# Performance work log

Measured on AMD Instinct MI355X. Metric: run time of the kernel, lower is better.

## Reference

```python
import jax, jax.numpy as jnp
import numpy as np

B = 4; C = 3; IMG = 256; P = 16; HP = 16; HW = 256
DIM = 512; DEPTH = 6; HEADS = 8; DH = 64
NS = 50; SH = 4; SDH = 64; ITERS = 3; RPD = 128; FF = 2048; N = NS + HW


def _ln(x, g, b):
    m = jnp.mean(x, -1, keepdims=True)
    v = jnp.var(x, -1, keepdims=True)
    return (x - m) * jax.lax.rsqrt(v + 1e-5) * g + b


def _rms(x, g):
    # lucidrains RMSNorm: F.normalize(x, dim=-1) * sqrt(dim) * gamma
    n = jnp.linalg.norm(x, axis=-1, keepdims=True)
    return x / jnp.maximum(n, 1e-12) * (DIM ** 0.5) * g


def setup_inputs() -> dict:
    key = jax.random.key(0)
    ks = iter(jax.random.split(key, 64))
    def W(*s):
        return jax.random.normal(next(ks), s, jnp.float32) * 0.02
    SI = SH * SDH
    d = {}
    d['images'] = jax.random.normal(next(ks), (B, C, IMG, IMG), jnp.float32)
    d['slot_noise'] = jax.random.normal(next(ks), (B, NS, DIM), jnp.float32)
    d['patch_w'] = W(C * P * P, DIM); d['patch_b'] = jnp.zeros((DIM,))
    d['hpos'] = W(HP, DIM); d['wpos'] = W(HP, DIM)
    d['rp_w1'] = W(2, RPD); d['rp_b1'] = jnp.zeros((RPD,))
    d['rp_w2'] = W(RPD, RPD); d['rp_b2'] = jnp.zeros((RPD,))
    d['rp_w3'] = W(RPD, HEADS); d['rp_b3'] = jnp.zeros((HEADS,))
    d['slots_mu'] = W(1, 1, DIM); d['slots_logsigma'] = jnp.zeros((1, 1, DIM))
    d['sa_ln_in_g'] = jnp.ones((DIM,)); d['sa_ln_in_b'] = jnp.zeros((DIM,))
    d['sa_ln_sl_g'] = jnp.ones((DIM,)); d['sa_ln_sl_b'] = jnp.zeros((DIM,))
    d['sa_wq'] = W(DIM, SI); d['sa_bq'] = jnp.zeros((SI,))
    d['sa_wk'] = W(DIM, SI); d['sa_bk'] = jnp.zeros((SI,))
    d['sa_wv'] = W(DIM, SI); d['sa_bv'] = jnp.zeros((SI,))
    d['sa_wo'] = W(SI, DIM); d['sa_bo'] = jnp.zeros((DIM,))
    d['gru_wih'] = W(DIM, 3 * DIM); d['gru_whh'] = W(DIM, 3 * DIM)
    d['gru_bih'] = jnp.zeros((3 * DIM,)); d['gru_bhh'] = jnp.zeros((3 * DIM,))
    d['sa_ln_ff_g'] = jnp.ones((DIM,)); d['sa_ln_ff_b'] = jnp.zeros((DIM,))
    d['sa_mlp_w1'] = W(DIM, DIM); d['sa_mlp_b1'] = jnp.zeros((DIM,))
    d['sa_mlp_w2'] = W(DIM, DIM); d['sa_mlp_b2'] = jnp.zeros((DIM,))
    d['s2c_w'] = W(DIM, 2); d['s2c_b'] = jnp.zeros((2,))
    d['attn_g'] = jnp.ones((DEPTH, DIM))
    d['wq'] = W(DEPTH, DIM, HEADS * DH); d['wk'] = W(DEPTH, DIM, HEADS * DH)
    d['wv'] = W(DEPTH, DIM, HEADS * DH); d['wo'] = W(DEPTH, HEADS * DH, DIM)
    d['ff_g'] = jnp.ones((DEPTH, DIM))
    d['ff_w1'] = W(DEPTH, DIM, FF); d['ff_b1'] = jnp.zeros((DEPTH, FF))
    d['ff_w2'] = W(DEPTH, FF, DIM); d['ff_b2'] = jnp.zeros((DEPTH, DIM))
    d['final_g'] = jnp.ones((DIM,))
    d['pred_w'] = W(DIM, DIM); d['pred_b'] = jnp.zeros((DIM,))
    return d


def reference(images, slot_noise, patch_w, patch_b, hpos, wpos,
              rp_w1, rp_b1, rp_w2, rp_b2, rp_w3, rp_b3,
              slots_mu, slots_logsigma, sa_ln_in_g, sa_ln_in_b, sa_ln_sl_g, sa_ln_sl_b,
              sa_wq, sa_bq, sa_wk, sa_bk, sa_wv, sa_bv, sa_wo, sa_bo,
              gru_wih, gru_whh, gru_bih, gru_bhh, sa_ln_ff_g, sa_ln_ff_b,
              sa_mlp_w1, sa_mlp_b1, sa_mlp_w2, sa_mlp_b2, s2c_w, s2c_b,
              attn_g, wq, wk, wv, wo, ff_g, ff_w1, ff_b1, ff_w2, ff_b2,
              final_g, pred_w, pred_b):
    b = images.shape[0]
    # patchify: b c (h p1) (w p2) -> b h w (p1 p2 c)
    x = images.reshape(b, C, HP, P, HP, P).transpose(0, 2, 4, 3, 5, 1).reshape(b, HP, HP, P * P * C)
    tokens = x @ patch_w + patch_b                     # [b, HP, HP, DIM]
    tokens = tokens + hpos[:, None, :] + wpos[None, :, :]
    tokens = tokens.reshape(b, HW, DIM)
    # --- multi-head slot attention ---
    inp = _ln(tokens, sa_ln_in_g, sa_ln_in_b)
    k = (inp @ sa_wk + sa_bk).reshape(b, HW, SH, SDH).transpose(0, 2, 1, 3)
    v = (inp @ sa_wv + sa_bv).reshape(b, HW, SH, SDH).transpose(0, 2, 1, 3)
    slots = slots_mu + jnp.exp(slots_logsigma) * slot_noise  # [b, NS, DIM]
    scale = SDH ** -0.5
    for _ in range(ITERS):
        prev = slots
        s = _ln(slots, sa_ln_sl_g, sa_ln_sl_b)
        q = (s @ sa_wq + sa_bq).reshape(b, NS, SH, SDH).transpose(0, 2, 1, 3)
        dots = jnp.einsum('bhid,bhjd->bhij', q, k) * scale     # [b, SH, NS, HW]
        attn = jax.nn.softmax(dots, axis=-2) + 1e-8            # softmax over slots
        attn = attn / jnp.sum(attn, -1, keepdims=True)         # weighted mean over inputs
        upd = jnp.einsum('bhij,bhjd->bhid', attn, v)
        upd = upd.transpose(0, 2, 1, 3).reshape(b, NS, SH * SDH) @ sa_wo + sa_bo
        # GRUCell(updates, prev_slots)
        gx = upd @ gru_wih + gru_bih
        gh = prev @ gru_whh + gru_bhh
        xr, xz, xn = jnp.split(gx, 3, -1)
        hr, hz, hn = jnp.split(gh, 3, -1)
        r = jax.nn.sigmoid(xr + hr)
        z = jax.nn.sigmoid(xz + hz)
        nn_ = jnp.tanh(xn + r * hn)
        slots = (1 - z) * nn_ + z * prev
        slots = slots + (jax.nn.relu(_ln(slots, sa_ln_ff_g, sa_ln_ff_b) @ sa_mlp_w1 + sa_mlp_b1) @ sa_mlp_w2 + sa_mlp_b2)
    objects = slots
    slot_coords = objects @ s2c_w + s2c_b              # [b, NS, 2]
    # --- relative position MLP bias (slots coords + patch grid) ---
    g = jnp.arange(HP, dtype=jnp.float32)
    grid = jnp.stack(jnp.meshgrid(g, g, indexing='ij'), -1).reshape(HW, 2)
    coords = jnp.concatenate([slot_coords, jnp.broadcast_to(grid, (b, HW, 2))], axis=1)  # [b, N, 2]
    rel = coords[:, :, None, :] - coords[:, None, :, :]   # [b, N, N, 2]
    hmid = jax.nn.silu(rel @ rp_w1 + rp_b1)
    hmid = jax.nn.silu(hmid @ rp_w2 + rp_b2)
    bias = jnp.transpose(hmid @ rp_w3 + rp_b3, (0, 3, 1, 2))  # [b, HEADS, N, N]
    # --- transformer with per-layer rel-pos bias ---
    x = jnp.concatenate([objects, tokens], axis=1)     # [b, N, DIM]
    ascale = DH ** -0.5
    for l in range(DEPTH):
        h = _rms(x, attn_g[l])
        qh = (h @ wq[l]).reshape(b, N, HEADS, DH).transpose(0, 2, 1, 3)
        kh = (h @ wk[l]).reshape(b, N, HEADS, DH).transpose(0, 2, 1, 3)
        vh = (h @ wv[l]).reshape(b, N, HEADS, DH).transpose(0, 2, 1, 3)
        sim = jnp.einsum('bhid,bhjd->bhij', qh, kh) * ascale + bias
        a = jax.nn.softmax(sim, -1)
        o = jnp.einsum('bhij,bhjd->bhid', a, vh).transpose(0, 2, 1, 3).reshape(b, N, HEADS * DH) @ wo[l]
        x = x + o
        h = _rms(x, ff_g[l])
        x = x + (jax.nn.gelu(h @ ff_w1[l] + ff_b1[l]) @ ff_w2[l] + ff_b2[l])
    x = _rms(x, final_g)
    return x[:, NS:] @ pred_w + pred_b                 # [b, HW, DIM]
```

## Files before the change

### kernel.cpp

```cpp
#include <hip/hip_runtime.h>
#include <hip/hip_bf16.h>

typedef __hip_bfloat16 bf16;
typedef short short8v __attribute__((ext_vector_type(8)));
typedef float float4v __attribute__((ext_vector_type(4)));

static __device__ __forceinline__ float b2f(bf16 x){ return __bfloat162float(x); }

static __device__ __forceinline__ float ldin(const void* p, size_t i, bool isbf) {
  return isbf ? b2f(((const bf16*)p)[i]) : ((const float*)p)[i];
}

static __device__ __forceinline__ unsigned short f2bu(float f) {
  bf16 h = __float2bfloat16(f);
  return *reinterpret_cast<unsigned short*>(&h);
}

#define CDIV(a,b) (((a)+(b)-1)/(b))

#define NB   4
#define NSL  50
#define HWT  256
#define NT   306
#define DIM  512
#define NH   8
#define FF   2048
#define RPP  28100
#define PCH  56200

static __device__ __forceinline__ void rp_decode(int q, int& i, int& j) {
  if (q < 15300) { i = q / NT; j = q % NT; }
  else { int r = q - 15300; i = NSL + r / NSL; j = r % NSL; }
}

__global__ void detect_k(const void* p, int* flag) {
  const unsigned short* u = (const unsigned short*)p;
  int t = threadIdx.x;
  int e = (u[t] >> 7) & 0xFF;
  __shared__ int anybad;
  if (t == 0) anybad = 0;
  __syncthreads();
  if (e >= 0x88) atomicOr(&anybad, 1);
  __syncthreads();
  if (t == 0) *flag = anybad ? 0 : 1;
}

struct WtArgs {
  const void* W[17];
  unsigned long long wto[17];
  int K[17], N[17];
  int base[18];
};

__global__ __launch_bounds__(256) void wtrans_all_k(WtArgs a, unsigned short* __restrict__ WT,
                                                    const int* __restrict__ flagp) {
  const bool isbf = *flagp != 0;
  int bid = blockIdx.x;
  int idx = 0;
#pragma unroll
  for (int i = 1; i < 17; ++i) if (bid >= a.base[i]) idx = i;
  int t0 = bid - a.base[idx];
  const int K = a.K[idx], N = a.N[idx];
  const int tilesN = N >> 6;
  const int perLayer = tilesN * (K >> 6);
  const int layer = t0 / perLayer, rem = t0 % perLayer;
  const int n0 = (rem % tilesN) * 64, k0 = (rem / tilesN) * 64;
  const void* W = a.W[idx];
  unsigned short* dst0 = WT + a.wto[idx];
  const size_t slice = (size_t)K * N * layer;

  __shared__ unsigned short S[64 * 72];
  int t = threadIdx.x;
  int kk = t >> 4, nn = (t & 15) * 4;
#pragma unroll
  for (int r = 0; r < 4; ++r) {
    int k = k0 + kk + r * 16;
    unsigned short v[4];
    if (isbf) {
      ushort4 u = *(const ushort4*)((const unsigned short*)W + slice + (size_t)k * N + n0 + nn);
      v[0]=u.x; v[1]=u.y; v[2]=u.z; v[3]=u.w;
    } else {
      float4 f = *(const float4*)((const float*)W + slice + (size_t)k * N + n0 + nn);
      v[0]=f2bu(f.x); v[1]=f2bu(f.y); v[2]=f2bu(f.z); v[3]=f2bu(f.w);
    }
#pragma unroll
    for (int i = 0; i < 4; ++i) S[(nn + i) * 72 + kk + r * 16] = v[i];
  }
  __syncthreads();
  int nr = t >> 2, kc = (t & 3) * 16;
  short8v s0 = *(const short8v*)&S[nr * 72 + kc];
  short8v s1 = *(const short8v*)&S[nr * 72 + kc + 8];
  unsigned short* dst = dst0 + slice + (size_t)(n0 + nr) * K + k0 + kc;
  *(short8v*)dst = s0;
  *(short8v*)(dst + 8) = s1;
}

#define LDK 72
static __device__ __forceinline__ void gemm_body2(
    const void* __restrict__ A, int aty,
    const unsigned short* __restrict__ WT,
    const void* __restrict__ bias, size_t boff,
    void* __restrict__ C, int oty,
    int M, int N, int K, int kbeg, int kend,
    int act, int mode, int spec,
    const void* __restrict__ p0, const void* __restrict__ p1,
    bool isbf)
{
  __shared__ unsigned short As[64 * LDK];
  __shared__ unsigned short Bs[64 * LDK];
  const int tid = threadIdx.x;
  const int lane = tid & 63, wave = tid >> 6;
  const int quad = lane >> 4, ti = lane & 15;
  const int wm = (wave & 1) * 32, wn = (wave >> 1) * 32;
  const int bm = blockIdx.y * 64, bn = blockIdx.x * 64;
  const int srow = tid >> 2, sch = (tid & 3) * 16;

  unsigned short ha[16], hb[16];
  const int gm = bm + srow;
  const bool aok = gm < M;
  const unsigned short* Abf = (const unsigned short*)A + (size_t)gm * K;
  const float*          Af  = (const float*)A + (size_t)gm * K;
  const unsigned short* Bp  = WT + (size_t)(bn + srow) * K;

  auto fetchA = [&](int k0) {
    if (aok) {
      if (aty) {
        const ushort4* ap = (const ushort4*)(Abf + k0 + sch);
#pragma unroll
        for (int i = 0; i < 4; ++i) {
          ushort4 u = ap[i];
          ha[i*4+0]=u.x; ha[i*4+1]=u.y; ha[i*4+2]=u.z; ha[i*4+3]=u.w;
        }
      } else {
        const float4* ap = (const float4*)(Af + k0 + sch);
#pragma unroll
        for (int i = 0; i < 4; ++i) {
          float4 f = ap[i];
          ha[i*4+0]=f2bu(f.x); ha[i*4+1]=f2bu(f.y); ha[i*4+2]=f2bu(f.z); ha[i*4+3]=f2bu(f.w);
        }
      }
    } else {
#pragma unroll
      for (int i = 0; i < 16; ++i) ha[i] = 0;
    }
  };
  auto fetchB = [&](int k0) {
    const ushort4* bp = (const ushort4*)(Bp + k0 + sch);
#pragma unroll
    for (int i = 0; i < 4; ++i) {
      ushort4 u = bp[i];
      hb[i*4+0]=u.x; hb[i*4+1]=u.y; hb[i*4+2]=u.z; hb[i*4+3]=u.w;
    }
  };

  float4v acc00 = {0,0,0,0}, acc01 = {0,0,0,0}, acc10 = {0,0,0,0}, acc11 = {0,0,0,0};
  fetchA(kbeg); fetchB(kbeg);
  for (int k0 = kbeg; k0 < kend; k0 += 64) {
    *(short8v*)&As[srow * LDK + sch]     = *(short8v*)ha;
    *(short8v*)&As[srow * LDK + sch + 8] = *(short8v*)(ha + 8);
    *(short8v*)&Bs[srow * LDK + sch]     = *(short8v*)hb;
    *(short8v*)&Bs[srow * LDK + sch + 8] = *(short8v*)(hb + 8);
    __syncthreads();
    if (k0 + 64 < kend) { fetchA(k0 + 64); fetchB(k0 + 64); }
#pragma unroll
    for (int ks = 0; ks < 2; ++ks) {
      short8v a0 = *reinterpret_cast<const short8v*>(&As[(wm + ti)      * LDK + ks * 32 + quad * 8]);
      short8v a1 = *reinterpret_cast<const short8v*>(&As[(wm + 16 + ti) * LDK + ks * 32 + quad * 8]);
      short8v b0 = *reinterpret_cast<const short8v*>(&Bs[(wn + ti)      * LDK + ks * 32 + quad * 8]);
      short8v b1 = *reinterpret_cast<const short8v*>(&Bs[(wn + 16 + ti) * LDK + ks * 32 + quad * 8]);
      acc00 = __builtin_amdgcn_mfma_f32_16x16x32_bf16(a0, b0, acc00, 0, 0, 0);
      acc01 = __builtin_amdgcn_mfma_f32_16x16x32_bf16(a0, b1, acc01, 0, 0, 0);
      acc10 = __builtin_amdgcn_mfma_f32_16x16x32_bf16(a1, b0, acc10, 0, 0, 0);
      acc11 = __builtin_amdgcn_mfma_f32_16x16x32_bf16(a1, b1, acc11, 0, 0, 0);
    }
    __syncthreads();
  }

  float4v accs[2][2] = {{acc00, acc01}, {acc10, acc11}};
#pragma unroll
  for (int mi = 0; mi < 2; ++mi) {
#pragma unroll
    for (int ni = 0; ni < 2; ++ni) {
      int row0 = bm + wm + mi * 16 + quad * 4;
      int col  = bn + wn + ni * 16 + ti;
      float bv = (bias && kbeg == 0) ? ldin(bias, boff + col, isbf) : 0.f;
#pragma unroll
      for (int r = 0; r < 4; ++r) {
        int row = row0 + r;
        if (row >= M) continue;
        float v = accs[mi][ni][r] + bv;
        if (act == 1) v = fmaxf(v, 0.f);
        else if (act == 2) {
          float u = 0.7978845608028654f * (v + 0.044715f * v * v * v);
          v = 0.5f * v * (1.f + tanhf(u));
        } else if (act == 3) {
          v = v / (1.f + expf(-v));
        }
        if (spec == 2 && kbeg == 0) {
          int hh = (row >> 4) & 15, ww = row & 15;
          v += ldin(p0, hh * N + col, isbf) + ldin(p1, ww * N + col, isbf);
        }
        if (spec == 1) {
          int b_ = row / NT, n_ = row % NT;
          if (n_ >= NSL) {
            size_t oi = ((size_t)(b_ * HWT + (n_ - NSL))) * N + col;
            if (isbf) ((bf16*)C)[oi] = __float2bfloat16(v);
            else      ((float*)C)[oi] = v;
          }
        } else {
          size_t idx = (size_t)row * N + col;
          if (oty) ((bf16*)C)[idx] = __float2bfloat16(v);
          else {
            float* Cf = (float*)C;
            if (mode == 2) atomicAdd(&Cf[idx], v);
            else if (mode == 1) Cf[idx] += v;
            else Cf[idx] = v;
          }
        }
      }
    }
  }
}

__global__ __launch_bounds__(256) void gemm_mfma(
    const void* A, int aty, const unsigned short* WT, size_t woff,
    const void* bias, size_t boff, void* C, int oty,
    int M, int N, int K, int act, int accum, int zsplit,
    int spec, const void* p0, const void* p1, const int* __restrict__ flagp)
{
  int ksz = K / zsplit;
  int kbeg = blockIdx.z * ksz;
  int mode = zsplit > 1 ? 2 : (accum ? 1 : 0);
  gemm_body2(A, aty, WT + woff, bias, boff, C, oty, M, N, K, kbeg, kbeg + ksz,
             act, mode, spec, p0, p1, *flagp != 0);
}

__global__ __launch_bounds__(256) void gemm_mfma_tri(
    const void* A, int aty, const unsigned short* WT, size_t o0, size_t o1, size_t o2,
    void* C0, void* C1, void* C2, int oty, int M, int N, int K,
    const int* __restrict__ flagp)
{
  size_t o = blockIdx.z == 0 ? o0 : (blockIdx.z == 1 ? o1 : o2);
  void* C = blockIdx.z == 0 ? C0 : (blockIdx.z == 1 ? C1 : C2);
  gemm_body2(A, aty, WT + o, nullptr, 0, C, oty, M, N, K, 0, K, 0, 0, 0,
             nullptr, nullptr, *flagp != 0);
}

__global__ __launch_bounds__(256) void gemm_mfma_duo(
    const void* A0, const void* A1, int aty, const unsigned short* WT, size_t o0, size_t o1,
    const void* bias0, const void* bias1, void* C0, void* C1, int oty,
    int M, int N, int K, const int* __restrict__ flagp)
{
  const void* A = blockIdx.z ? A1 : A0;
  size_t o = blockIdx.z ? o1 : o0;
  const void* bias = blockIdx.z ? bias1 : bias0;
  void* C = blockIdx.z ? C1 : C0;
  gemm_body2(A, aty, WT + o, bias, 0, C, oty, M, N, K, 0, K, 0, 0, 0,
             nullptr, nullptr, *flagp != 0);
}

__global__ void coords_k(const float* __restrict__ slots, const void* __restrict__ w,
                         const void* __restrict__ bv, float* __restrict__ coords,
                         const int* __restrict__ flagp) {
  const bool isbf = *flagp != 0;
  __shared__ float r0[256], r1[256];
  int blk = blockIdx.x, t = threadIdx.x;
  if (blk < 200) {
    int b = blk / 50, n = blk % 50;
    const float* x = slots + (size_t)blk * DIM;
    float v0 = x[t], v1 = x[t + 256];
    float a0 = v0 * ldin(w, 2 * t, isbf)     + v1 * ldin(w, 2 * (t + 256), isbf);
    float a1 = v0 * ldin(w, 2 * t + 1, isbf) + v1 * ldin(w, 2 * (t + 256) + 1, isbf);
    r0[t] = a0; r1[t] = a1;
    __syncthreads();
    for (int o = 128; o > 0; o >>= 1) {
      if (t < o) { r0[t] += r0[t + o]; r1[t] += r1[t + o]; }
      __syncthreads();
    }
    if (t == 0) {
      coords[((size_t)b * NT + n) * 2]     = r0[0] + ldin(bv, 0, isbf);
      coords[((size_t)b * NT + n) * 2 + 1] = r1[0] + ldin(bv, 1, isbf);
    }
  } else {
#pragma unroll
    for (int s = 0; s < 4; ++s) {
      int i = t + 256 * s;
      int b = i >> 8, tt = i & 255;
      coords[((size_t)b * NT + NSL + tt) * 2]     = (float)(tt >> 4);
      coords[((size_t)b * NT + NSL + tt) * 2 + 1] = (float)(tt & 15);
    }
  }
}

__global__ void patchify_k(const void* __restrict__ img, unsigned short* __restrict__ xp,
                           const int* __restrict__ flagp) {
  const bool isbf = *flagp != 0;
  int i = blockIdx.x * 256 + threadIdx.x;
  if (i >= NB * HWT * 768) return;
  int col = i % 768, row = i / 768;
  int c = col % 3, p2 = (col / 3) & 15, p1 = col / 48;
  int w = row & 15, h = (row >> 4) & 15, b = row >> 8;
  xp[i] = f2bu(ldin(img, (((size_t)(b * 3 + c) * 256 + h * 16 + p1) * 256) + w * 16 + p2, isbf));
}

__global__ void ln512_k(const float* __restrict__ X, const void* __restrict__ g,
                        const void* __restrict__ b, unsigned short* __restrict__ Y,
                        const int* __restrict__ flagp) {
  const bool isbf = *flagp != 0;
  int row = blockIdx.x, t = threadIdx.x;
  const float* x = X + (size_t)row * DIM;
  float v0 = x[t], v1 = x[t + 256];
  __shared__ float rs[256], rq[256];
  rs[t] = v0 + v1; rq[t] = v0 * v0 + v1 * v1;
  __syncthreads();
  for (int o = 128; o > 0; o >>= 1) {
    if (t < o) { rs[t] += rs[t + o]; rq[t] += rq[t + o]; }
    __syncthreads();
  }
  float mean = rs[0] * (1.f / 512.f);
  float var  = rq[0] * (1.f / 512.f) - mean * mean;
  float inv  = rsqrtf(var + 1e-5f);
  unsigned short* y = Y + (size_t)row * DIM;
  y[t]       = f2bu((v0 - mean) * inv * ldin(g, t, isbf)       + ldin(b, t, isbf));
  y[t + 256] = f2bu((v1 - mean) * inv * ldin(g, t + 256, isbf) + ldin(b, t + 256, isbf));
}

__global__ void rms512_k(const float* __restrict__ X, const void* __restrict__ g,
                         int goff, unsigned short* __restrict__ Y, const int* __restrict__ flagp) {
  const bool isbf = *flagp != 0;
  int row = blockIdx.x, t = threadIdx.x;
  const float* x = X + (size_t)row * DIM;
  float v0 = x[t], v1 = x[t + 256];
  __shared__ float rq[256];
  rq[t] = v0 * v0 + v1 * v1;
  __syncthreads();
  for (int o = 128; o > 0; o >>= 1) {
    if (t < o) rq[t] += rq[t + o];
    __syncthreads();
  }
  float nrm = sqrtf(rq[0]);
  float sc = 22.62741699796952f / fmaxf(nrm, 1e-12f);
  unsigned short* y = Y + (size_t)row * DIM;
  y[t]       = f2bu(v0 * sc * ldin(g, goff + t, isbf));
  y[t + 256] = f2bu(v1 * sc * ldin(g, goff + t + 256, isbf));
}

__global__ void slots_init_k(const void* __restrict__ mu, const void* __restrict__ ls,
                             const void* __restrict__ noise, float* __restrict__ slots,
                             const int* __restrict__ flagp) {
  const bool isbf = *flagp != 0;
  int i = blockIdx.x * 256 + threadIdx.x;
  if (i >= NB * NSL * DIM) return;
  int d = i & 511;
  slots[i] = ldin(mu, d, isbf) + expf(ldin(ls, d, isbf)) * ldin(noise, i, isbf);
}

__global__ void slot_dots_k(const float* __restrict__ q, const float* __restrict__ k,
                            float* __restrict__ dots) {
  int blk = blockIdx.x;
  int i = blk % 50, h = (blk / 50) & 3, b = blk / 200;
  int j = threadIdx.x;
  __shared__ float qs[64];
  if (threadIdx.x < 64) qs[threadIdx.x] = q[((size_t)(b * 50 + i)) * 256 + h * 64 + threadIdx.x];
  __syncthreads();
  const float* kr = k + ((size_t)(b * 256 + j)) * 256 + h * 64;
  float s = 0.f;
#pragma unroll 8
  for (int d = 0; d < 64; ++d) s = fmaf(qs[d], kr[d], s);
  dots[(((size_t)(b * 4 + h) * 50) + i) * 256 + j] = s * 0.125f;
}

__global__ __launch_bounds__(256) void sm_renorm_k(float* __restrict__ att) {
  __shared__ float S[NSL * 257];
  const int t = threadIdx.x;
  float* base = att + (size_t)blockIdx.x * (NSL * HWT);
  float v[NSL];
#pragma unroll
  for (int i = 0; i < NSL; ++i) v[i] = base[i * HWT + t];
  float m = -1e30f;
#pragma unroll
  for (int i = 0; i < NSL; ++i) m = fmaxf(m, v[i]);
  float s = 0.f;
#pragma unroll
  for (int i = 0; i < NSL; ++i) { float e = __expf(v[i] - m); v[i] = e; s += e; }
  float inv = 1.f / s;
#pragma unroll
  for (int i = 0; i < NSL; ++i) S[i * 257 + t] = fmaf(v[i], inv, 1e-8f);
  __syncthreads();
  const int w = t >> 6, l = t & 63;
  for (int r = w; r < NSL; r += 4) {
    float a0 = S[r * 257 + l],        a1 = S[r * 257 + 64 + l];
    float a2 = S[r * 257 + 128 + l],  a3 = S[r * 257 + 192 + l];
    float s4 = a0 + a1 + a2 + a3;
#pragma unroll
    for (int o = 1; o < 64; o <<= 1) s4 += __shfl_xor(s4, o);
    float inv2 = 1.f / s4;
    base[r * HWT + l]       = a0 * inv2;
    base[r * HWT + 64 + l]  = a1 * inv2;
    base[r * HWT + 128 + l] = a2 * inv2;
    base[r * HWT + 192 + l] = a3 * inv2;
  }
}

__global__ void slot_upd_k(const float* __restrict__ attn, const float* __restrict__ v,
                           float* __restrict__ upd) {
  int bi = blockIdx.x;
  int b = bi / 50, i = bi % 50;
  int t = threadIdx.x, h = t >> 6;
  const float* arow = attn + ((size_t)((b * 4 + h) * 50) + i) * 256;
  float s = 0.f;
  for (int j = 0; j < 256; ++j) s = fmaf(arow[j], v[((size_t)(b * 256 + j)) * 256 + t], s);
  upd[(size_t)bi * 256 + t] = s;
}

__global__ void gru_k(const float* __restrict__ gx, const float* __restrict__ gh,
                      float* __restrict__ slots) {
  int i = blockIdx.x * 256 + threadIdx.x;
  if (i >= NB * NSL * DIM) return;
  int row = i >> 9, d = i & 511;
  size_t b3 = (size_t)row * 1536;
  float xr = gx[b3 + d], xz = gx[b3 + 512 + d], xn = gx[b3 + 1024 + d];
  float hr = gh[b3 + d], hz = gh[b3 + 512 + d], hn = gh[b3 + 1024 + d];
  float r = 1.f / (1.f + expf(-(xr + hr)));
  float z = 1.f / (1.f + expf(-(xz + hz)));
  float n = tanhf(xn + r * hn);
  float prev = slots[i];
  slots[i] = (1.f - z) * n + z * prev;
}

__global__ void relpos_table_k(const void* w1, const void* b1, const void* w2,
                               const void* b2, const void* w3, const void* b3,
                               float* __restrict__ tab, const int* __restrict__ flagp) {
  const bool isbf = *flagp != 0;
  int blk = blockIdx.x;
  float r0 = (float)(blk / 31 - 15), r1 = (float)(blk % 31 - 15);
  int t = threadIdx.x;
  __shared__ float h1[128], h2[128];
  float a = fmaf(r0, ldin(w1, t, isbf), fmaf(r1, ldin(w1, 128 + t, isbf), ldin(b1, t, isbf)));
  h1[t] = a / (1.f + expf(-a));
  __syncthreads();
  float s = ldin(b2, t, isbf);
#pragma unroll 4
  for (int k = 0; k < 128; ++k) s = fmaf(h1[k], ldin(w2, k * 128 + t, isbf), s);
  h2[t] = s / (1.f + expf(-s));
  __syncthreads();
  if (t < 8) {
    float o = ldin(b3, t, isbf);
#pragma unroll 4
    for (int k = 0; k < 128; ++k) o = fmaf(h2[k], ldin(w3, k * 8 + t, isbf), o);
    tab[blk * 8 + t] = o;
  }
}

__global__ void bias_fill_k(const float* __restrict__ tab, float* __restrict__ bias) {
  int i = blockIdx.x * 256 + threadIdx.x;
  if (i >= NB * NH * HWT * HWT) return;
  int jj = i & 255, ii = (i >> 8) & 255, h = (i >> 16) & 7, b = i >> 19;
  int di = (ii >> 4) - (jj >> 4) + 15;
  int dj = (ii & 15) - (jj & 15) + 15;
  bias[(((size_t)(b * NH + h) * NT) + NSL + ii) * NT + NSL + jj] = tab[(di * 31 + dj) * 8 + h];
}

__global__ void rp_l1_k(const float* __restrict__ coords, const void* w1, const void* b1,
                        unsigned short* __restrict__ H, int pbase, int pcount,
                        const int* __restrict__ flagp) {
  const bool isbf = *flagp != 0;
  int idx = blockIdx.x * 256 + threadIdx.x;
  if (idx >= pcount * 128) return;
  int pl = idx >> 7, u = idx & 127;
  int p = pbase + pl;
  int q = p % RPP, bb = p / RPP;
  int ii, jj;
  rp_decode(q, ii, jj);
  float r0 = coords[(bb * NT + ii) * 2]     - coords[(bb * NT + jj) * 2];
  float r1 = coords[(bb * NT + ii) * 2 + 1] - coords[(bb * NT + jj) * 2 + 1];
  float a = fmaf(r0, ldin(w1, u, isbf), fmaf(r1, ldin(w1, 128 + u, isbf), ldin(b1, u, isbf)));
  H[(size_t)pl * 128 + u] = f2bu(a / (1.f + expf(-a)));
}

__global__ __launch_bounds__(256) void rp_l3_k(
    const unsigned short* __restrict__ H2, const void* w3, const void* b3,
    float* __restrict__ bias, int pbase, int pcount, const int* __restrict__ flagp) {
  const bool isbf = *flagp != 0;
  __shared__ float W3s[8 * 132];
  int t = threadIdx.x;
  for (int e = t; e < 1024; e += 256) {
    int k = e >> 3, hh = e & 7;
    W3s[hh * 132 + k] = ldin(w3, e, isbf);
  }
  __syncthreads();
  int pl = blockIdx.x * 32 + (t >> 3), hh = t & 7;
  if (pl >= pcount) return;
  int p = pbase + pl;
  int q = p % RPP, bb = p / RPP;
  int ii, jj;
  rp_decode(q, ii, jj);
  float s = ldin(b3, hh, isbf);
  const unsigned short* hrow = H2 + (size_t)pl * 128;
  const float* wrow = &W3s[hh * 132];
#pragma unroll 8
  for (int k4 = 0; k4 < 32; ++k4) {
    ushort4 h4 = *(const ushort4*)(hrow + k4 * 4);
    float4  w4 = *(const float4*)(wrow + k4 * 4);
    s = fmaf(b2f(*reinterpret_cast<bf16*>(&h4.x)), w4.x, s);
    s = fmaf(b2f(*reinterpret_cast<bf16*>(&h4.y)), w4.y, s);
    s = fmaf(b2f(*reinterpret_cast<bf16*>(&h4.z)), w4.z, s);
    s = fmaf(b2f(*reinterpret_cast<bf16*>(&h4.w)), w4.w, s);
  }
  bias[((size_t)(bb * NH + hh) * NT + ii) * NT + jj] = s;
}

__global__ void build_x_k(const float* __restrict__ slots, const float* __restrict__ tok,
                          float* __restrict__ x) {
  int i = blockIdx.x * 256 + threadIdx.x;
  if (i >= NB * NT * DIM) return;
  int d = i & 511, n = (i >> 9) % NT, b = i / (NT * DIM);
  x[i] = (n < NSL) ? slots[((size_t)(b * NSL + n)) * DIM + d]
                   : tok[((size_t)(b * HWT + (n - NSL))) * DIM + d];
}

__global__ __launch_bounds__(256) void attn_fused_k(
    const unsigned short* __restrict__ Qb, const unsigned short* __restrict__ Kb,
    const unsigned short* __restrict__ Vb, const float* __restrict__ bias,
    unsigned short* __restrict__ Ob)
{
  const int bh = blockIdx.y, b = bh >> 3, h = bh & 7;
  const int i0 = blockIdx.x * 32;
  __shared__ unsigned short Qs[32 * 72];
  __shared__ unsigned short Ks[64 * 72];
  __shared__ float S[32 * 332];
  unsigned short* P = (unsigned short*)S;

  const int tid = threadIdx.x;
  const int lane = tid & 63, wave = tid >> 6, quad = lane >> 4, ti = lane & 15;
  const int mi = wave & 1, nh = wave >> 1;

  {
    int r = tid >> 3, c = (tid & 7) * 8;
    int gi = i0 + r;
    ushort4 u0 = {0,0,0,0}, u1 = {0,0,0,0};
    if (gi < NT) {
      const ushort4* p = (const ushort4*)(Qb + ((size_t)(b * NT + gi)) * DIM + h * 64 + c);
      u0 = p[0]; u1 = p[1];
    }
    *(ushort4*)&Qs[r * 72 + c] = u0;
    *(ushort4*)&Qs[r * 72 + c + 4] = u1;
  }

  for (int kt = 0; kt < 5; ++kt) {
    __syncthreads();
    {
      int kr = tid >> 2, c = (tid & 3) * 16;
      int gj = kt * 64 + kr;
      ushort4 v[4] = {{0,0,0,0},{0,0,0,0},{0,0,0,0},{0,0,0,0}};
      if (gj < NT) {
        const ushort4* p = (const ushort4*)(Kb + ((size_t)(b * NT + gj)) * DIM + h * 64 + c);
#pragma unroll
        for (int i = 0; i < 4; ++i) v[i] = p[i];
      }
#pragma unroll
      for (int i = 0; i < 4; ++i) *(ushort4*)&Ks[kr * 72 + c + i * 4] = v[i];
    }
    __syncthreads();
#pragma unroll
    for (int ntl = 0; ntl < 2; ++ntl) {
      int nt = nh * 2 + ntl;
      float4v acc = {0,0,0,0};
#pragma unroll
      for (int ks = 0; ks < 2; ++ks) {
        short8v a  = *(const short8v*)&Qs[(mi * 16 + ti) * 72 + ks * 32 + quad * 8];
        short8v bb = *(const short8v*)&Ks[(nt * 16 + ti) * 72 + ks * 32 + quad * 8];
        acc = __builtin_amdgcn_mfma_f32_16x16x32_bf16(a, bb, acc, 0, 0, 0);
      }
      int colL = kt * 64 + nt * 16 + ti;
      int row0 = mi * 16 + quad * 4;
#pragma unroll
      for (int r = 0; r < 4; ++r) {
        int row_g = i0 + row0 + r;
        float val;
        if (colL < NT) {
          float bv = (row_g < NT) ? bias[((size_t)bh * NT + row_g) * NT + colL] : 0.f;
          val = acc[r] * 0.125f + bv;
        } else val = -1e30f;
        S[(row0 + r) * 332 + colL] = val;
      }
    }
  }
  __syncthreads();

  {
    int rl = tid >> 3, sub = tid & 7;
    float sv[40];
#pragma unroll
    for (int k = 0; k < 40; ++k) sv[k] = S[rl * 332 + sub + k * 8];
    float m = -1e30f;
#pragma unroll
    for (int k = 0; k < 40; ++k) m = fmaxf(m, sv[k]);
    m = fmaxf(m, __shfl_xor(m, 1));
    m = fmaxf(m, __shfl_xor(m, 2));
    m = fmaxf(m, __shfl_xor(m, 4));
    float s = 0.f;
#pragma unroll
    for (int k = 0; k < 40; ++k) { float e = __expf(sv[k] - m); sv[k] = e; s += e; }
    s += __shfl_xor(s, 1);
    s += __shfl_xor(s, 2);
    s += __shfl_xor(s, 4);
    float inv = 1.f / s;
    __syncthreads();
#pragma unroll
    for (int k = 0; k < 40; ++k) P[rl * 664 + sub + k * 8] = f2bu(sv[k] * inv);
  }

  float4v oacc[2] = {{0,0,0,0},{0,0,0,0}};
  for (int vt = 0; vt < 5; ++vt) {
    __syncthreads();
    {
      int key = tid & 63, d0 = (tid >> 6) * 16;
      int gj = vt * 64 + key;
      unsigned short hv[16];
      if (gj < NT) {
        const ushort4* p = (const ushort4*)(Vb + ((size_t)(b * NT + gj)) * DIM + h * 64 + d0);
#pragma unroll
        for (int i = 0; i < 4; ++i) {
          ushort4 u = p[i];
          hv[i*4+0]=u.x; hv[i*4+1]=u.y; hv[i*4+2]=u.z; hv[i*4+3]=u.w;
        }
      } else {
#pragma unroll
        for (int i = 0; i < 16; ++i) hv[i] = 0;
      }
#pragma unroll
      for (int i = 0; i < 16; ++i) Ks[(d0 + i) * 72 + key] = hv[i];
    }
    __syncthreads();
#pragma unroll
    for (int ntl = 0; ntl < 2; ++ntl) {
      int nt = nh * 2 + ntl;
#pragma unroll
      for (int ks = 0; ks < 2; ++ks) {
        short8v a  = *(const short8v*)&P[(mi * 16 + ti) * 664 + vt * 64 + ks * 32 + quad * 8];
        short8v bb = *(const short8v*)&Ks[(nt * 16 + ti) * 72 + ks * 32 + quad * 8];
        oacc[ntl] = __builtin_amdgcn_mfma_f32_16x16x32_bf16(a, bb, oacc[ntl], 0, 0, 0);
      }
    }
  }

#pragma unroll
  for (int ntl = 0; ntl < 2; ++ntl) {
    int dim = nh * 32 + ntl * 16 + ti;
#pragma unroll
    for (int r = 0; r < 4; ++r) {
      int row_g = i0 + mi * 16 + quad * 4 + r;
      if (row_g < NT)
        Ob[((size_t)(b * NT + row_g)) * DIM + h * 64 + dim] = f2bu(oacc[ntl][r]);
    }
  }
}

extern "C" void kernel_launch(void* const* d_in, const int* in_sizes, int n_in,
                              void* d_out, int out_size, void* d_ws, size_t ws_size,
                              hipStream_t stream) {
  const void* images        = d_in[0];
  const void* slot_noise    = d_in[1];
  const void* patch_w       = d_in[2];
  const void* patch_b       = d_in[3];
  const void* hpos          = d_in[4];
  const void* wpos          = d_in[5];
  const void* rp_w1         = d_in[6];
  const void* rp_b1         = d_in[7];
  const void* rp_w2         = d_in[8];
  const void* rp_b2         = d_in[9];
  const void* rp_w3         = d_in[10];
  const void* rp_b3         = d_in[11];
  const void* slots_mu      = d_in[12];
  const void* slots_logsig  = d_in[13];
  const void* sa_ln_in_g    = d_in[14];
  const void* sa_ln_in_b    = d_in[15];
  const void* sa_ln_sl_g    = d_in[16];
  const void* sa_ln_sl_b    = d_in[17];
  const void* sa_wq         = d_in[18];
  const void* sa_bq         = d_in[19];
  const void* sa_wk         = d_in[20];
  const void* sa_bk         = d_in[21];
  const void* sa_wv         = d_in[22];
  const void* sa_bv         = d_in[23];
  const void* sa_wo         = d_in[24];
  const void* sa_bo         = d_in[25];
  const void* gru_wih       = d_in[26];
  const void* gru_whh       = d_in[27];
  const void* gru_bih       = d_in[28];
  const void* gru_bhh       = d_in[29];
  const void* sa_ln_ff_g    = d_in[30];
  const void* sa_ln_ff_b    = d_in[31];
  const void* sa_mlp_w1     = d_in[32];
  const void* sa_mlp_b1     = d_in[33];
  const void* sa_mlp_w2     = d_in[34];
  const void* sa_mlp_b2     = d_in[35];
  const void* s2c_w         = d_in[36];
  const void* s2c_b         = d_in[37];
  const void* attn_g        = d_in[38];
  const void* wq            = d_in[39];
  const void* wk            = d_in[40];
  const void* wv            = d_in[41];
  const void* wo            = d_in[42];
  const void* ff_g          = d_in[43];
  const void* ff_w1         = d_in[44];
  const void* ff_b1         = d_in[45];
  const void* ff_w2         = d_in[46];
  const void* ff_b2         = d_in[47];
  const void* final_g       = d_in[48];
  const void* pred_w        = d_in[49];
  const void* pred_b        = d_in[50];

  float* ws = (float*)d_ws;
  int* FLAG = (int*)ws;
  size_t off = 16;
  auto alloc = [&](size_t n) { float* p = ws + off; off += (n + 15) & ~(size_t)15; return p; };
  float* TOK   = alloc((size_t)NB * HWT * DIM);
  unsigned short* INPB = (unsigned short*)alloc((size_t)NB * HWT * DIM / 2);
  float* KB    = alloc((size_t)NB * HWT * 256);
  float* VB    = alloc((size_t)NB * HWT * 256);
  float* SLOTS = alloc((size_t)NB * NSL * DIM);
  unsigned short* SLNB = (unsigned short*)alloc((size_t)NB * NSL * DIM / 2);
  float* QB    = alloc((size_t)NB * NSL * 256);
  float* ATT   = alloc((size_t)NB * 4 * NSL * HWT);
  float* UPD   = alloc((size_t)NB * NSL * 256);
  float* UPDP  = alloc((size_t)NB * NSL * DIM);
  unsigned short* HIDSB = (unsigned short*)alloc((size_t)NB * NSL * DIM / 2);
  float* CRD   = alloc((size_t)NB * NT * 2);
  float* TAB   = alloc((size_t)961 * 8);
  float* BIAS  = alloc((size_t)NB * NH * NT * NT);
  float* X     = alloc((size_t)NB * NT * DIM);
  unsigned short* HBB  = (unsigned short*)alloc((size_t)NB * NT * DIM / 2);
  unsigned short* QHB  = (unsigned short*)alloc((size_t)NB * NT * DIM / 2);
  unsigned short* KHB  = (unsigned short*)alloc((size_t)NB * NT * DIM / 2);
  unsigned short* VHB  = (unsigned short*)alloc((size_t)NB * NT * DIM / 2);
  float* SIM   = alloc((size_t)NB * NH * NT * NT);
  unsigned short* OBB  = (unsigned short*)alloc((size_t)NB * NT * DIM / 2);
  unsigned short* FFHB = (unsigned short*)alloc((size_t)NB * NT * FF / 2);
  float* OUTT  = alloc((size_t)NB * NT * DIM);
  unsigned short* XPB = (unsigned short*)OUTT;
  float* GX = SIM;
  float* GH = SIM + (size_t)NB * NSL * 1536;
  const size_t oPatch = 0;
  const size_t oKw    = oPatch + (size_t)512 * 768;
  const size_t oVw    = oKw    + (size_t)256 * 512;
  const size_t oQw    = oVw    + (size_t)256 * 512;
  const size_t oWo    = oQw    + (size_t)256 * 512;
  const size_t oGih   = oWo    + (size_t)512 * 256;
  const size_t oGhh   = oGih   + (size_t)1536 * 512;
  const size_t oMlp1  = oGhh   + (size_t)1536 * 512;
  const size_t oMlp2  = oMlp1  + (size_t)512 * 512;
  const size_t oRp2   = oMlp2  + (size_t)512 * 512;
  const size_t oWq    = oRp2   + (size_t)128 * 128;
  const size_t oWk    = oWq    + (size_t)6 * 512 * 512;
  const size_t oWv    = oWk    + (size_t)6 * 512 * 512;
  const size_t oWol   = oWv    + (size_t)6 * 512 * 512;
  const size_t oFf1   = oWol   + (size_t)6 * 512 * 512;
  const size_t oFf2   = oFf1   + (size_t)6 * 512 * 2048;
  const size_t oPred  = oFf2   + (size_t)6 * 2048 * 512;
  const size_t wtTotal = oPred + (size_t)512 * 512;
  unsigned short* WTS = (unsigned short*)alloc((wtTotal + 1) / 2);
  (void)ws_size; (void)in_sizes; (void)n_in; (void)out_size;

#define GEMMM(A_, ATY_, WOFF_, BIAS_, BOFF_, C_, OTY_, M_, N_, K_, ACT_, ACC_, ZS_, SPEC_, P0_, P1_) \
  gemm_mfma<<<dim3((N_)/64, CDIV((M_),64), (ZS_)), 256, 0, stream>>>( \
      A_, ATY_, WTS, (size_t)(WOFF_), BIAS_, (size_t)(BOFF_), C_, OTY_, M_, N_, K_, ACT_, ACC_, ZS_, \
      SPEC_, P0_, P1_, FLAG)

  const int MROW = NB * NT;
  const int MS   = NB * NSL;

  detect_k<<<1, 256, 0, stream>>>(images, FLAG);
  {
    WtArgs a;
    const void* Wp[17] = { patch_w, sa_wk, sa_wv, sa_wq, sa_wo, gru_wih, gru_whh,
                           sa_mlp_w1, sa_mlp_w2, rp_w2, wq, wk, wv, wo, ff_w1, ff_w2, pred_w };
    const size_t Oo[17] = { oPatch, oKw, oVw, oQw, oWo, oGih, oGhh,
                            oMlp1, oMlp2, oRp2, oWq, oWk, oWv, oWol, oFf1, oFf2, oPred };
    const int Kk[17] = {768,512,512,512,256,512,512,512,512,128,512,512,512,512,512,2048,512};
    const int Nn[17] = {512,256,256,256,512,1536,1536,512,512,128,512,512,512,512,2048,512,512};
    const int Ll[17] = {1,1,1,1,1,1,1,1,1,1,6,6,6,6,6,6,1};
    int acc = 0;
    for (int i = 0; i < 17; ++i) {
      a.W[i] = Wp[i]; a.wto[i] = Oo[i]; a.K[i] = Kk[i]; a.N[i] = Nn[i];
      a.base[i] = acc;
      acc += Ll[i] * (Kk[i] >> 6) * (Nn[i] >> 6);
    }
    a.base[17] = acc;
    wtrans_all_k<<<acc, 256, 0, stream>>>(a, WTS, FLAG);
  }

  patchify_k<<<CDIV(NB*HWT*768, 256), 256, 0, stream>>>(images, XPB, FLAG);
  GEMMM(XPB, 1, oPatch, patch_b, 0, TOK, 0, NB*HWT, DIM, 768, 0, 0, 1, 2, hpos, wpos);

  ln512_k<<<NB*HWT, 256, 0, stream>>>(TOK, sa_ln_in_g, sa_ln_in_b, INPB, FLAG);
  gemm_mfma_duo<<<dim3(4, 16, 2), 256, 0, stream>>>(
      INPB, INPB, 1, WTS, oKw, oVw, sa_bk, sa_bv, KB, VB, 0, NB*HWT, 256, DIM, FLAG);
  slots_init_k<<<CDIV(NB*NSL*DIM, 256), 256, 0, stream>>>(slots_mu, slots_logsig, slot_noise, SLOTS, FLAG);

  for (int it = 0; it < 3; ++it) {
    ln512_k<<<MS, 256, 0, stream>>>(SLOTS, sa_ln_sl_g, sa_ln_sl_b, SLNB, FLAG);
    GEMMM(SLNB, 1, oQw, sa_bq, 0, QB, 0, MS, 256, DIM, 0, 0, 1, 0, nullptr, nullptr);
    slot_dots_k<<<NB*4*NSL, 256, 0, stream>>>(QB, KB, ATT);
    sm_renorm_k<<<16, 256, 0, stream>>>(ATT);
    slot_upd_k<<<MS, 256, 0, stream>>>(ATT, VB, UPD);
    GEMMM(UPD, 0, oWo, sa_bo, 0, UPDP, 0, MS, DIM, 256, 0, 0, 1, 0, nullptr, nullptr);
    gemm_mfma_duo<<<dim3(24, 4, 2), 256, 0, stream>>>(
        UPDP, SLOTS, 0, WTS, oGih, oGhh, gru_bih, gru_bhh, GX, GH, 0, MS, 1536, DIM, FLAG);
    gru_k<<<CDIV(NB*NSL*DIM, 256), 256, 0, stream>>>(GX, GH, SLOTS);
    ln512_k<<<MS, 256, 0, stream>>>(SLOTS, sa_ln_ff_g, sa_ln_ff_b, SLNB, FLAG);
    GEMMM(SLNB, 1, oMlp1, sa_mlp_b1, 0, HIDSB, 1, MS, DIM, DIM, 1, 0, 1, 0, nullptr, nullptr);
    GEMMM(HIDSB, 1, oMlp2, sa_mlp_b2, 0, SLOTS, 0, MS, DIM, DIM, 0, 1, 1, 0, nullptr, nullptr);
  }

  coords_k<<<201, 256, 0, stream>>>(SLOTS, s2c_w, s2c_b, CRD, FLAG);
  relpos_table_k<<<961, 128, 0, stream>>>(rp_w1, rp_b1, rp_w2, rp_b2, rp_w3, rp_b3, TAB, FLAG);
  bias_fill_k<<<CDIV(NB*NH*HWT*HWT, 256), 256, 0, stream>>>(TAB, BIAS);
  {
    unsigned short* H1 = HBB;
    unsigned short* H2 = HBB + (size_t)PCH * 128;
    for (int c = 0; c < 2; ++c) {
      int pb = c * PCH;
      rp_l1_k<<<CDIV(PCH*128, 256), 256, 0, stream>>>(CRD, rp_w1, rp_b1, H1, pb, PCH, FLAG);
      GEMMM(H1, 1, oRp2, rp_b2, 0, H2, 1, PCH, 128, 128, 3, 0, 1, 0, nullptr, nullptr);
      rp_l3_k<<<CDIV(PCH,32), 256, 0, stream>>>(H2, rp_w3, rp_b3, BIAS, pb, PCH, FLAG);
    }
  }

  build_x_k<<<CDIV(NB*NT*DIM, 256), 256, 0, stream>>>(SLOTS, TOK, X);
  for (int l = 0; l < 6; ++l) {
    size_t lw = (size_t)l * 512 * 512;
    rms512_k<<<MROW, 256, 0, stream>>>(X, attn_g, l * DIM, HBB, FLAG);
    gemm_mfma_tri<<<dim3(8, 20, 3), 256, 0, stream>>>(
        HBB, 1, WTS, oWq + lw, oWk + lw, oWv + lw, QHB, KHB, VHB, 1, MROW, DIM, DIM, FLAG);
    attn_fused_k<<<dim3(10, NB*NH), 256, 0, stream>>>(QHB, KHB, VHB, BIAS, OBB);
    GEMMM(OBB, 1, oWol + lw, (const void*)nullptr, 0, X, 0, MROW, DIM, DIM, 0, 1, 2, 0, nullptr, nullptr);
    rms512_k<<<MROW, 256, 0, stream>>>(X, ff_g, l * DIM, HBB, FLAG);
    GEMMM(HBB, 1, oFf1 + (size_t)l * 512 * 2048, ff_b1, l * FF, FFHB, 1, MROW, FF, DIM, 2, 0, 1, 0, nullptr, nullptr);
    GEMMM(FFHB, 1, oFf2 + (size_t)l * 2048 * 512, ff_b2, l * DIM, X, 0, MROW, DIM, FF, 0, 1, 4, 0, nullptr, nullptr);
  }

  rms512_k<<<MROW, 256, 0, stream>>>(X, final_g, 0, HBB, FLAG);
  GEMMM(HBB, 1, oPred, pred_b, 0, d_out, 0, MROW, DIM, DIM, 0, 0, 1, 1, nullptr, nullptr);

#undef GEMMM
}
```

Measured before the change: 1.186 ms.

## Fuse GRU with LayerNorm, compute relpos bias on the fly, split softmax renorm

The patch-to-patch relative-position bias is now looked up from a small per-head table held in shared memory inside the attention kernel, so the large bias_fill pass over BIAS is dropped. The GRU update and the following LayerNorm are fused into one per-row kernel. The slot softmax no longer does a two-phase renormalisation in 16 blocks; the row renormalisation is folded into slot_upd_k as a scaling factor. The patch-embedding GEMM switches to a 3-way split-K with atomic adds after a memset of its output, and the GEMM epilogue is moved into a helper function. These changes cut launches and memory traffic, at the cost of extra index arithmetic in attention and atomic accumulation in the patch GEMM.

```diff
diff --git a/kernel.cpp b/kernel.cpp
--- a/kernel.cpp
+++ b/kernel.cpp
@@ -93,6 +93,52 @@
   unsigned short* dst = dst0 + slice + (size_t)(n0 + nr) * K + k0 + kc;
   *(short8v*)dst = s0;
   *(short8v*)(dst + 8) = s1;
+}
+
+static __device__ __forceinline__ void gemm_epi(
+    float4v accv, int row0, int col,
+    const void* __restrict__ bias, size_t boff,
+    void* __restrict__ C, int oty,
+    int M, int N, int kbeg,
+    int act, int mode, int spec,
+    const void* __restrict__ p0, const void* __restrict__ p1,
+    bool isbf)
+{
+  float bv = (bias && kbeg == 0) ? ldin(bias, boff + col, isbf) : 0.f;
+#pragma unroll
+  for (int r = 0; r < 4; ++r) {
+    int row = row0 + r;
+    if (row >= M) continue;
+    float v = accv[r] + bv;
+    if (act == 1) v = fmaxf(v, 0.f);
+    else if (act == 2) {
+      float u = 0.7978845608028654f * (v + 0.044715f * v * v * v);
+      v = 0.5f * v * (1.f + tanhf(u));
+    } else if (act == 3) {
+      v = v / (1.f + expf(-v));
+    }
+    if (spec == 2 && kbeg == 0) {
+      int hh = (row >> 4) & 15, ww = row & 15;
+      v += ldin(p0, hh * N + col, isbf) + ldin(p1, ww * N + col, isbf);
+    }
+    if (spec == 1) {
+      int b_ = row / NT, n_ = row % NT;
+      if (n_ >= NSL) {
+        size_t oi = ((size_t)(b_ * HWT + (n_ - NSL))) * N + col;
+        if (isbf) ((bf16*)C)[oi] = __float2bfloat16(v);
+        else      ((float*)C)[oi] = v;
+      }
+    } else {
+      size_t idx = (size_t)row * N + col;
+      if (oty) ((bf16*)C)[idx] = __float2bfloat16(v);
+      else {
+        float* Cf = (float*)C;
+        if (mode == 2) atomicAdd(&Cf[idx], v);
+        else if (mode == 1) Cf[idx] += v;
+        else Cf[idx] = v;
+      }
+    }
+  }
 }
 
 #define LDK 72
@@ -178,48 +224,11 @@
 
   float4v accs[2][2] = {{acc00, acc01}, {acc10, acc11}};
 #pragma unroll
-  for (int mi = 0; mi < 2; ++mi) {
-#pragma unroll
-    for (int ni = 0; ni < 2; ++ni) {
-      int row0 = bm + wm + mi * 16 + quad * 4;
-      int col  = bn + wn + ni * 16 + ti;
-      float bv = (bias && kbeg == 0) ? ldin(bias, boff + col, isbf) : 0.f;
-#pragma unroll
-      for (int r = 0; r < 4; ++r) {
-        int row = row0 + r;
-        if (row >= M) continue;
-        float v = accs[mi][ni][r] + bv;
-        if (act == 1) v = fmaxf(v, 0.f);
-        else if (act == 2) {
-          float u = 0.7978845608028654f * (v + 0.044715f * v * v * v);
-          v = 0.5f * v * (1.f + tanhf(u));
-        } else if (act == 3) {
-          v = v / (1.f + expf(-v));
-        }
-        if (spec == 2 && kbeg == 0) {
-          int hh = (row >> 4) & 15, ww = row & 15;
-          v += ldin(p0, hh * N + col, isbf) + ldin(p1, ww * N + col, isbf);
-        }
-        if (spec == 1) {
-          int b_ = row / NT, n_ = row % NT;
-          if (n_ >= NSL) {
-            size_t oi = ((size_t)(b_ * HWT + (n_ - NSL))) * N + col;
-            if (isbf) ((bf16*)C)[oi] = __float2bfloat16(v);
-            else      ((float*)C)[oi] = v;
-          }
-        } else {
-          size_t idx = (size_t)row * N + col;
-          if (oty) ((bf16*)C)[idx] = __float2bfloat16(v);
-          else {
-            float* Cf = (float*)C;
-            if (mode == 2) atomicAdd(&Cf[idx], v);
-            else if (mode == 1) Cf[idx] += v;
-            else Cf[idx] = v;
-          }
-        }
-      }
-    }
-  }
+  for (int mi = 0; mi < 2; ++mi)
+#pragma unroll
+    for (int ni = 0; ni < 2; ++ni)
+      gemm_epi(accs[mi][ni], bm + wm + mi * 16 + quad * 4, bn + wn + ni * 16 + ti,
+               bias, boff, C, oty, M, N, kbeg, act, mode, spec, p0, p1, isbf);
 }
 
 __global__ __launch_bounds__(256) void gemm_mfma(
@@ -370,13 +379,14 @@
   dots[(((size_t)(b * 4 + h) * 50) + i) * 256 + j] = s * 0.125f;
 }
 
-__global__ __launch_bounds__(256) void sm_renorm_k(float* __restrict__ att) {
-  __shared__ float S[NSL * 257];
-  const int t = threadIdx.x;
-  float* base = att + (size_t)blockIdx.x * (NSL * HWT);
+__global__ void colsm_k(float* __restrict__ dots) {
+  int idx = blockIdx.x * 256 + threadIdx.x;
+  if (idx >= 4096) return;
+  int j = idx & 255, bh = idx >> 8;
+  float* base = dots + ((size_t)bh * NSL) * 256 + j;
   float v[NSL];
 #pragma unroll
-  for (int i = 0; i < NSL; ++i) v[i] = base[i * HWT + t];
+  for (int i = 0; i < NSL; ++i) v[i] = base[i * 256];
   float m = -1e30f;
 #pragma unroll
   for (int i = 0; i < NSL; ++i) m = fmaxf(m, v[i]);
@@ -385,47 +395,58 @@
   for (int i = 0; i < NSL; ++i) { float e = __expf(v[i] - m); v[i] = e; s += e; }
   float inv = 1.f / s;
 #pragma unroll
-  for (int i = 0; i < NSL; ++i) S[i * 257 + t] = fmaf(v[i], inv, 1e-8f);
-  __syncthreads();
-  const int w = t >> 6, l = t & 63;
-  for (int r = w; r < NSL; r += 4) {
-    float a0 = S[r * 257 + l],        a1 = S[r * 257 + 64 + l];
-    float a2 = S[r * 257 + 128 + l],  a3 = S[r * 257 + 192 + l];
-    float s4 = a0 + a1 + a2 + a3;
-#pragma unroll
-    for (int o = 1; o < 64; o <<= 1) s4 += __shfl_xor(s4, o);
-    float inv2 = 1.f / s4;
-    base[r * HWT + l]       = a0 * inv2;
-    base[r * HWT + 64 + l]  = a1 * inv2;
-    base[r * HWT + 128 + l] = a2 * inv2;
-    base[r * HWT + 192 + l] = a3 * inv2;
-  }
+  for (int i = 0; i < NSL; ++i) base[i * 256] = fmaf(v[i], inv, 1e-8f);
 }
 
 __global__ void slot_upd_k(const float* __restrict__ attn, const float* __restrict__ v,
                            float* __restrict__ upd) {
   int bi = blockIdx.x;
   int b = bi / 50, i = bi % 50;
-  int t = threadIdx.x, h = t >> 6;
+  int t = threadIdx.x, h = t >> 6, lane = t & 63;
   const float* arow = attn + ((size_t)((b * 4 + h) * 50) + i) * 256;
+  float s4 = arow[lane] + arow[lane + 64] + arow[lane + 128] + arow[lane + 192];
+#pragma unroll
+  for (int o = 1; o < 64; o <<= 1) s4 += __shfl_xor(s4, o);
+  float inv = 1.f / s4;
   float s = 0.f;
   for (int j = 0; j < 256; ++j) s = fmaf(arow[j], v[((size_t)(b * 256 + j)) * 256 + t], s);
-  upd[(size_t)bi * 256 + t] = s;
-}
-
-__global__ void gru_k(const float* __restrict__ gx, const float* __restrict__ gh,
-                      float* __restrict__ slots) {
-  int i = blockIdx.x * 256 + threadIdx.x;
-  if (i >= NB * NSL * DIM) return;
-  int row = i >> 9, d = i & 511;
+  upd[(size_t)bi * 256 + t] = s * inv;
+}
+
+__global__ __launch_bounds__(256) void gruln_k(
+    const float* __restrict__ gx, const float* __restrict__ gh,
+    float* __restrict__ slots, const void* __restrict__ g, const void* __restrict__ bb,
+    unsigned short* __restrict__ Y, const int* __restrict__ flagp) {
+  const bool isbf = *flagp != 0;
+  int row = blockIdx.x, t = threadIdx.x;
   size_t b3 = (size_t)row * 1536;
-  float xr = gx[b3 + d], xz = gx[b3 + 512 + d], xn = gx[b3 + 1024 + d];
-  float hr = gh[b3 + d], hz = gh[b3 + 512 + d], hn = gh[b3 + 1024 + d];
-  float r = 1.f / (1.f + expf(-(xr + hr)));
-  float z = 1.f / (1.f + expf(-(xz + hz)));
-  float n = tanhf(xn + r * hn);
-  float prev = slots[i];
-  slots[i] = (1.f - z) * n + z * prev;
+  float s01[2];
+#pragma unroll
+  for (int half = 0; half < 2; ++half) {
+    int d = t + half * 256;
+    float xr = gx[b3 + d], xz = gx[b3 + 512 + d], xn = gx[b3 + 1024 + d];
+    float hr = gh[b3 + d], hz = gh[b3 + 512 + d], hn = gh[b3 + 1024 + d];
+    float r = 1.f / (1.f + expf(-(xr + hr)));
+    float z = 1.f / (1.f + expf(-(xz + hz)));
+    float n = tanhf(xn + r * hn);
+    float prev = slots[(size_t)row * DIM + d];
+    s01[half] = (1.f - z) * n + z * prev;
+    slots[(size_t)row * DIM + d] = s01[half];
+  }
+  __shared__ float rs[256], rq[256];
+  rs[t] = s01[0] + s01[1];
+  rq[t] = s01[0] * s01[0] + s01[1] * s01[1];
+  __syncthreads();
+  for (int o = 128; o > 0; o >>= 1) {
+    if (t < o) { rs[t] += rs[t + o]; rq[t] += rq[t + o]; }
+    __syncthreads();
+  }
+  float mean = rs[0] * (1.f / 512.f);
+  float var  = rq[0] * (1.f / 512.f) - mean * mean;
+  float inv  = rsqrtf(var + 1e-5f);
+  unsigned short* y = Y + (size_t)row * DIM;
+  y[t]       = f2bu((s01[0] - mean) * inv * ldin(g, t, isbf)       + ldin(bb, t, isbf));
+  y[t + 256] = f2bu((s01[1] - mean) * inv * ldin(g, t + 256, isbf) + ldin(bb, t + 256, isbf));
 }
 
 __global__ void relpos_table_k(const void* w1, const void* b1, const void* w2,
@@ -450,15 +471,6 @@
     for (int k = 0; k < 128; ++k) o = fmaf(h2[k], ldin(w3, k * 8 + t, isbf), o);
     tab[blk * 8 + t] = o;
   }
-}
-
-__global__ void bias_fill_k(const float* __restrict__ tab, float* __restrict__ bias) {
-  int i = blockIdx.x * 256 + threadIdx.x;
-  if (i >= NB * NH * HWT * HWT) return;
-  int jj = i & 255, ii = (i >> 8) & 255, h = (i >> 16) & 7, b = i >> 19;
-  int di = (ii >> 4) - (jj >> 4) + 15;
-  int dj = (ii & 15) - (jj & 15) + 15;
-  bias[(((size_t)(b * NH + h) * NT) + NSL + ii) * NT + NSL + jj] = tab[(di * 31 + dj) * 8 + h];
 }
 
 __global__ void rp_l1_k(const float* __restrict__ coords, const void* w1, const void* b1,
@@ -522,18 +534,21 @@
 __global__ __launch_bounds__(256) void attn_fused_k(
     const unsigned short* __restrict__ Qb, const unsigned short* __restrict__ Kb,
     const unsigned short* __restrict__ Vb, const float* __restrict__ bias,
-    unsigned short* __restrict__ Ob)
+    const float* __restrict__ tab, unsigned short* __restrict__ Ob)
 {
   const int bh = blockIdx.y, b = bh >> 3, h = bh & 7;
   const int i0 = blockIdx.x * 32;
   __shared__ unsigned short Qs[32 * 72];
   __shared__ unsigned short Ks[64 * 72];
   __shared__ float S[32 * 332];
+  __shared__ float TabS[961];
   unsigned short* P = (unsigned short*)S;
 
   const int tid = threadIdx.x;
   const int lane = tid & 63, wave = tid >> 6, quad = lane >> 4, ti = lane & 15;
   const int mi = wave & 1, nh = wave >> 1;
+
+  for (int e = tid; e < 961; e += 256) TabS[e] = tab[e * 8 + h];
 
   {
     int r = tid >> 3, c = (tid & 7) * 8;
@@ -579,7 +594,17 @@
         int row_g = i0 + row0 + r;
         float val;
         if (colL < NT) {
-          float bv = (row_g < NT) ? bias[((size_t)bh * NT + row_g) * NT + colL] : 0.f;
+          float bv = 0.f;
+          if (row_g < NT) {
+            if (row_g >= NSL && colL >= NSL) {
+              int ii = row_g - NSL, jj = colL - NSL;
+              int di = (ii >> 4) - (jj >> 4) + 15;
+              int dj = (ii & 15) - (jj & 15) + 15;
+              bv = TabS[di * 31 + dj];
+            } else {
+              bv = bias[((size_t)bh * NT + row_g) * NT + colL];
+            }
+          }
           val = acc[r] * 0.125f + bv;
         } else val = -1e30f;
         S[(row0 + r) * 332 + colL] = val;
@@ -792,7 +817,8 @@
   }
 
   patchify_k<<<CDIV(NB*HWT*768, 256), 256, 0, stream>>>(images, XPB, FLAG);
-  GEMMM(XPB, 1, oPatch, patch_b, 0, TOK, 0, NB*HWT, DIM, 768, 0, 0, 1, 2, hpos, wpos);
+  hipMemsetAsync(TOK, 0, (size_t)NB * HWT * DIM * sizeof(float), stream);
+  GEMMM(XPB, 1, oPatch, patch_b, 0, TOK, 0, NB*HWT, DIM, 768, 0, 0, 3, 2, hpos, wpos);
 
   ln512_k<<<NB*HWT, 256, 0, stream>>>(TOK, sa_ln_in_g, sa_ln_in_b, INPB, FLAG);
   gemm_mfma_duo<<<dim3(4, 16, 2), 256, 0, stream>>>(
@@ -803,20 +829,18 @@
     ln512_k<<<MS, 256, 0, stream>>>(SLOTS, sa_ln_sl_g, sa_ln_sl_b, SLNB, FLAG);
     GEMMM(SLNB, 1, oQw, sa_bq, 0, QB, 0, MS, 256, DIM, 0, 0, 1, 0, nullptr, nullptr);
     slot_dots_k<<<NB*4*NSL, 256, 0, stream>>>(QB, KB, ATT);
-    sm_renorm_k<<<16, 256, 0, stream>>>(ATT);
+    colsm_k<<<16, 256, 0, stream>>>(ATT);
     slot_upd_k<<<MS, 256, 0, stream>>>(ATT, VB, UPD);
     GEMMM(UPD, 0, oWo, sa_bo, 0, UPDP, 0, MS, DIM, 256, 0, 0, 1, 0, nullptr, nullptr);
     gemm_mfma_duo<<<dim3(24, 4, 2), 256, 0, stream>>>(
         UPDP, SLOTS, 0, WTS, oGih, oGhh, gru_bih, gru_bhh, GX, GH, 0, MS, 1536, DIM, FLAG);
-    gru_k<<<CDIV(NB*NSL*DIM, 256), 256, 0, stream>>>(GX, GH, SLOTS);
-    ln512_k<<<MS, 256, 0, stream>>>(SLOTS, sa_ln_ff_g, sa_ln_ff_b, SLNB, FLAG);
+    gruln_k<<<MS, 256, 0, stream>>>(GX, GH, SLOTS, sa_ln_ff_g, sa_ln_ff_b, SLNB, FLAG);
     GEMMM(SLNB, 1, oMlp1, sa_mlp_b1, 0, HIDSB, 1, MS, DIM, DIM, 1, 0, 1, 0, nullptr, nullptr);
     GEMMM(HIDSB, 1, oMlp2, sa_mlp_b2, 0, SLOTS, 0, MS, DIM, DIM, 0, 1, 1, 0, nullptr, nullptr);
   }
 
   coords_k<<<201, 256, 0, stream>>>(SLOTS, s2c_w, s2c_b, CRD, FLAG);
   relpos_table_k<<<961, 128, 0, stream>>>(rp_w1, rp_b1, rp_w2, rp_b2, rp_w3, rp_b3, TAB, FLAG);
-  bias_fill_k<<<CDIV(NB*NH*HWT*HWT, 256), 256, 0, stream>>>(TAB, BIAS);
   {
     unsigned short* H1 = HBB;
     unsigned short* H2 = HBB + (size_t)PCH * 128;
@@ -834,7 +858,7 @@
     rms512_k<<<MROW, 256, 0, stream>>>(X, attn_g, l * DIM, HBB, FLAG);
     gemm_mfma_tri<<<dim3(8, 20, 3), 256, 0, stream>>>(
         HBB, 1, WTS, oWq + lw, oWk + lw, oWv + lw, QHB, KHB, VHB, 1, MROW, DIM, DIM, FLAG);
-    attn_fused_k<<<dim3(10, NB*NH), 256, 0, stream>>>(QHB, KHB, VHB, BIAS, OBB);
+    attn_fused_k<<<dim3(10, NB*NH), 256, 0, stream>>>(QHB, KHB, VHB, BIAS, TAB, OBB);
     GEMMM(OBB, 1, oWol + lw, (const void*)nullptr, 0, X, 0, MROW, DIM, DIM, 0, 1, 2, 0, nullptr, nullptr);
     rms512_k<<<MROW, 256, 0, stream>>>(X, ff_g, l * DIM, HBB, FLAG);
     GEMMM(HBB, 1, oFf1 + (size_t)l * 512 * 2048, ff_b1, l * FF, FFHB, 1, MROW, FF, DIM, 2, 0, 1, 0, nullptr, nullptr);
```

Measured after the change: 1.158 ms. 2.3% less time.
